# Kernel optimization log

Hardware: AMD Instinct MI355X
Metric: run time of the kernel (lower is better)

## Reference

```python
import jax, jax.numpy as jnp
import numpy as np
from jax import lax

V, E, H = 32000, 256, 512
B, S_SRC, S_TGT = 32, 128, 64


def setup_inputs() -> dict:
    key = jax.random.key(0)
    ks = jax.random.split(key, 16)
    n = lambda k, shp: jax.random.normal(k, shp, dtype=jnp.float32) * 0.05
    return {
        "src": jax.random.randint(ks[0], (B, S_SRC), 0, V, dtype=jnp.int32),
        "tgt": jax.random.randint(ks[1], (B, S_TGT), 0, V, dtype=jnp.int32),
        "enc_emb": n(ks[2], (V, E)),
        "enc_Wih": n(ks[3], (4 * H, E)),
        "enc_Whh": n(ks[4], (4 * H, H)),
        "enc_b": n(ks[5], (4 * H,)),
        "attn_W": n(ks[6], (H, 2 * H)),
        "attn_b": n(ks[7], (H,)),
        "attn_v": jax.random.uniform(ks[8], (H,), dtype=jnp.float32),
        "dec_emb": n(ks[9], (V, E)),
        "dec_Wih": n(ks[10], (4 * H, E + H)),
        "dec_Whh": n(ks[11], (4 * H, H)),
        "dec_b": n(ks[12], (4 * H,)),
        "out_W": n(ks[13], (V, H)),
        "out_b": n(ks[14], (V,)),
    }


def _lstm_cell(x, h, c, Wih, Whh, b):
    # PyTorch gate order: i, f, g, o. b = b_ih + b_hh fused.
    z = x @ Wih.T + h @ Whh.T + b  # [B, 4H]
    i, f, g, o = jnp.split(z, 4, axis=-1)
    c_new = jax.nn.sigmoid(f) * c + jax.nn.sigmoid(i) * jnp.tanh(g)
    h_new = jax.nn.sigmoid(o) * jnp.tanh(c_new)
    return h_new, c_new


def reference(src, tgt, enc_emb, enc_Wih, enc_Whh, enc_b, attn_W, attn_b,
              attn_v, dec_emb, dec_Wih, dec_Whh, dec_b, out_W, out_b):
    b = src.shape[0]
    h0 = jnp.zeros((b, H), dtype=enc_emb.dtype)
    c0 = jnp.zeros((b, H), dtype=enc_emb.dtype)

    # ---- Encoder: single-layer LSTM over src ----
    emb_src = enc_emb[src]  # [B, S_src, E]

    def enc_step(carry, x_t):
        h, c = carry
        h, c = _lstm_cell(x_t, h, c, enc_Wih, enc_Whh, enc_b)
        return (h, c), h

    (h, c), enc_out = lax.scan(enc_step, (h0, c0), emb_src.transpose(1, 0, 2))
    enc_out = enc_out.transpose(1, 0, 2)  # [B, S_src, H]

    # attn_W acts on cat([hidden, enc]); split into hidden and encoder parts.
    W_h = attn_W[:, :H]   # [H, H]
    W_e = attn_W[:, H:]   # [H, H]
    enc_proj = jnp.einsum('bsh,kh->bsk', enc_out, W_e)  # precomputed [B, S, H]

    # ---- Decoder with per-step Bahdanau attention ----
    emb_tgt = dec_emb[tgt].transpose(1, 0, 2)  # [T, B, E]

    def dec_step(carry, e_t):
        h, c = carry
        energy = jnp.tanh(enc_proj + (h @ W_h.T + attn_b)[:, None, :])  # [B,S,H]
        score = energy @ attn_v                                          # [B,S]
        a = jax.nn.softmax(score, axis=1)
        context = jnp.einsum('bs,bsh->bh', a, enc_out)                   # [B,H]
        x = jnp.concatenate([e_t, context], axis=-1)                     # [B,E+H]
        h, c = _lstm_cell(x, h, c, dec_Wih, dec_Whh, dec_b)
        return (h, c), h

    _, dec_h = lax.scan(dec_step, (h, c), emb_tgt)
    dec_h = dec_h.transpose(1, 0, 2)  # [B, T, H]

    return dec_h @ out_W.T + out_b  # [B, T, V]
```

## Files before the change

### kernel.cpp

```cpp
#include <hip/hip_runtime.h>

#define B_    32
#define SSRC  128
#define STGT  64
#define E_    256
#define H_    512
#define G4    2048
#define V_    32000

typedef unsigned short u16;
typedef unsigned long long u64b;
typedef short bf16x8 __attribute__((ext_vector_type(8)));
typedef float f32x4 __attribute__((ext_vector_type(4)));

__device__ __forceinline__ u16 f2b(float f) {
  unsigned u = __float_as_uint(f);
  u += 0x7FFFu + ((u >> 16) & 1u);
  return (u16)(u >> 16);
}
__device__ __forceinline__ float b2f(u16 h) {
  return __uint_as_float(((unsigned)h) << 16);
}
__device__ __forceinline__ unsigned pk2(float lo, float hi) {
  return (unsigned)f2b(lo) | (((unsigned)f2b(hi)) << 16);
}
__device__ __forceinline__ float sigm(float x) { return 1.0f / (1.0f + __expf(-x)); }
__device__ __forceinline__ float tanh_(float x) { return 1.0f - 2.0f / (1.0f + __expf(2.0f * x)); }

#if defined(__has_builtin)
#if __has_builtin(__builtin_amdgcn_fdot2_f32_bf16)
#define HAS_DOT2 1
#endif
#endif
#ifdef HAS_DOT2
typedef __bf16 b162 __attribute__((ext_vector_type(2)));
__device__ __forceinline__ float dot2u(unsigned a, unsigned b, float acc) {
  return __builtin_amdgcn_fdot2_f32_bf16(__builtin_bit_cast(b162, a),
                                         __builtin_bit_cast(b162, b), acc, false);
}
#else
__device__ __forceinline__ float dot2u(unsigned a, unsigned b, float acc) {
  acc += __uint_as_float(a << 16) * __uint_as_float(b << 16);
  acc += __uint_as_float(a & 0xffff0000u) * __uint_as_float(b & 0xffff0000u);
  return acc;
}
#endif
__device__ __forceinline__ float dot4(uint4 w, uint4 h, float acc) {
  return dot2u(w.w, h.w, dot2u(w.z, h.z, dot2u(w.y, h.y, dot2u(w.x, h.x, acc))));
}

__device__ __forceinline__ int swz64(int c) {
  return (c & ~3) | ((c & 3) ^ ((c >> 3) & 3));
}

__device__ __forceinline__ uint4 cload4(const void* p) {
  uint4 r;
  asm volatile("global_load_dwordx4 %0, %1, off sc0 sc1\n\ts_waitcnt vmcnt(0)"
               : "=&v"(r) : "v"(p) : "memory");
  return r;
}
__device__ __forceinline__ void cstoref(float* p, float v) {
  asm volatile("global_store_dword %0, %1, off sc0 sc1" :: "v"(p), "v"(v) : "memory");
}
__device__ __forceinline__ void cstoreu(unsigned* p, unsigned v) {
  asm volatile("global_store_dword %0, %1, off sc0 sc1" :: "v"(p), "v"(v) : "memory");
}
__device__ __forceinline__ float cloadf_relaxed(const float* p) {
  return __hip_atomic_load(p, __ATOMIC_RELAXED, __HIP_MEMORY_SCOPE_AGENT);
}

__device__ __forceinline__ void arrive(int* flags, int myid, int target) {
  asm volatile("s_waitcnt vmcnt(0)" ::: "memory");
  __syncthreads();
  if (threadIdx.x == 0)
    __hip_atomic_store(flags + myid, target, __ATOMIC_RELAXED, __HIP_MEMORY_SCOPE_AGENT);
}
__device__ __forceinline__ void waitbar(int* flags, int target) {
  if (threadIdx.x < 64) {
    int l = threadIdx.x & 31;
    while (__hip_atomic_load(flags + l, __ATOMIC_RELAXED, __HIP_MEMORY_SCOPE_AGENT) < target)
      __builtin_amdgcn_s_sleep(1);
  }
  __syncthreads();
  asm volatile("" ::: "memory");
}

__global__ void prep_kernel(const int* __restrict__ src, const int* __restrict__ tgt,
                            const float* __restrict__ enc_emb, const float* __restrict__ dec_emb,
                            const float* __restrict__ enc_Wih, const float* __restrict__ dec_Wih,
                            const float* __restrict__ out_W,
                            u16* __restrict__ A_enc, u16* __restrict__ A_dec,
                            u16* __restrict__ WihE, u16* __restrict__ WihD,
                            u16* __restrict__ WihC, u16* __restrict__ outWb)
{
  const long n_outw = (long)V_ * H_;
  const long n_aenc = (long)B_ * SSRC * E_;
  const long n_adec = (long)B_ * STGT * E_;
  const long n_wih  = (long)G4 * E_;
  const long n_wcp  = (long)G4 * H_;
  const long total = n_outw + n_aenc + n_adec + 2 * n_wih + n_wcp;
  for (long i = (long)blockIdx.x * blockDim.x + threadIdx.x; i < total;
       i += (long)gridDim.x * blockDim.x) {
    long x = i;
    if (x < n_outw) { outWb[x] = f2b(out_W[x]); continue; }
    x -= n_outw;
    if (x < n_aenc) {
      int row = (int)(x >> 8), e = (int)(x & 255);
      A_enc[x] = f2b(enc_emb[(size_t)src[row] * E_ + e]);
      continue;
    }
    x -= n_aenc;
    if (x < n_adec) {
      int row = (int)(x >> 8), e = (int)(x & 255);
      A_dec[x] = f2b(dec_emb[(size_t)tgt[row] * E_ + e]);
      continue;
    }
    x -= n_adec;
    if (x < n_wih) { WihE[x] = f2b(enc_Wih[x]); continue; }
    x -= n_wih;
    if (x < n_wih) {
      int r = (int)(x >> 8), e = (int)(x & 255);
      WihD[x] = f2b(dec_Wih[(size_t)r * 768 + e]);
      continue;
    }
    x -= n_wih;
    {
      int r = (int)(x >> 9), k = (int)(x & 511);
      WihC[x] = f2b(dec_Wih[(size_t)r * 768 + 256 + k]);
    }
  }
}

template<int KTOT, bool OBF>
__global__ __launch_bounds__(256, 2) void gemm_nt(
    const u16* __restrict__ A, const u16* __restrict__ Bm,
    const float* __restrict__ bias, void* __restrict__ Cv, int M, int N)
{
  int nbm = M >> 7;
  int bn = blockIdx.x / nbm;
  int bm = blockIdx.x % nbm;
  int w = threadIdx.x >> 6, l = threadIdx.x & 63;
  int wr = w >> 1, wc = w & 1;
  int m0 = bm * 128 + wr * 64, n0 = bn * 128 + wc * 64;
  int lr = l & 15, ko = (l >> 4) * 8;
  f32x4 acc[4][4] = {};
  const u16* Ap = A + (size_t)(m0 + lr) * KTOT + ko;
  const u16* Bp = Bm + (size_t)(n0 + lr) * KTOT + ko;
  for (int k0 = 0; k0 < KTOT; k0 += 32) {
    bf16x8 af[4], bfr[4];
#pragma unroll
    for (int i = 0; i < 4; ++i) af[i] = *(const bf16x8*)(Ap + (size_t)i * 16 * KTOT + k0);
#pragma unroll
    for (int i = 0; i < 4; ++i) bfr[i] = *(const bf16x8*)(Bp + (size_t)i * 16 * KTOT + k0);
#pragma unroll
    for (int i = 0; i < 4; ++i)
#pragma unroll
      for (int j = 0; j < 4; ++j)
        acc[i][j] = __builtin_amdgcn_mfma_f32_16x16x32_bf16(af[i], bfr[j], acc[i][j], 0, 0, 0);
  }
  int rbase = (l >> 4) * 4;
#pragma unroll
  for (int i = 0; i < 4; ++i) {
#pragma unroll
    for (int j = 0; j < 4; ++j) {
      int gn = n0 + j * 16 + lr;
      float bv = bias[gn];
#pragma unroll
      for (int r = 0; r < 4; ++r) {
        int gm = m0 + i * 16 + rbase + r;
        float v = acc[i][j][r] + bv;
        if (OBF) ((u16*)Cv)[(size_t)gm * N + gn] = f2b(v);
        else     ((float*)Cv)[(size_t)gm * N + gn] = v;
      }
    }
  }
}

__device__ __forceinline__ void zgemv64(int tid, const uint4* Wu, const uint4* Hu,
                                        float (*part)[64][4]) {
  int rq = tid >> 4, kq = tid & 15;
  float acc[4][4] = {};
#pragma unroll
  for (int u = 0; u < 4; ++u) {
    int sc = swz64(kq * 4 + u);
    uint4 h0 = Hu[sc], h1 = Hu[64 + sc], h2 = Hu[128 + sc], h3 = Hu[192 + sc];
#pragma unroll
    for (int r = 0; r < 4; ++r) {
      uint4 wv = Wu[(rq * 4 + r) * 64 + sc];
      acc[r][0] = dot4(wv, h0, acc[r][0]);
      acc[r][1] = dot4(wv, h1, acc[r][1]);
      acc[r][2] = dot4(wv, h2, acc[r][2]);
      acc[r][3] = dot4(wv, h3, acc[r][3]);
    }
  }
#pragma unroll
  for (int r = 0; r < 4; ++r) {
    float4 v = {acc[r][0], acc[r][1], acc[r][2], acc[r][3]};
    *(float4*)&part[kq][(rq * 4 + r) ^ (kq & 7)][0] = v;
  }
}

template<typename GrowF>
__device__ __forceinline__ void fillw64(int tid, const float* Wsrc, uint4* Wu, GrowF grow) {
#pragma unroll 4
  for (int i = 0; i < 16; ++i) {
    int idx4 = tid + i * 256;
    int row = idx4 >> 6, c = idx4 & 63;
    const float* s = Wsrc + (size_t)grow(row) * 512 + c * 8;
    float4 a = *(const float4*)s, b4 = *(const float4*)(s + 4);
    uint4 pkv = {pk2(a.x, a.y), pk2(a.z, a.w), pk2(b4.x, b4.y), pk2(b4.z, b4.w)};
    Wu[row * 64 + swz64(c)] = pkv;
  }
}

__global__ __launch_bounds__(256, 1) void encoder_kernel(
    const float* __restrict__ enc_Whh, const float* __restrict__ attn_W,
    const u16* __restrict__ WihC, const u16* __restrict__ encXW,
    unsigned* __restrict__ h16buf, float* __restrict__ cfin,
    u16* __restrict__ eprojb, u16* __restrict__ eoPw, int* __restrict__ bars)
{
  const int tid = threadIdx.x;
  const int g = blockIdx.x & 7;
  const int gb = blockIdx.x >> 3;
  const int b0 = g * 4;
  const int ds0 = gb * 16;
  int* flags = bars + g * 64;

  __shared__ uint4 encW4[64 * 64];
  __shared__ uint4 web4[16 * 64];
  __shared__ uint4 hl16[4 * 64];
  __shared__ float part[16][64][4];
  __shared__ float zx[4][64];
  __shared__ float cS[4][16];

  if (tid < 64) cS[tid >> 4][tid & 15] = 0.f;
  fillw64(tid, enc_Whh, encW4, [&](int row) { return (row >> 4) * 512 + ds0 + (row & 15); });
#pragma unroll
  for (int i = 0; i < 4; ++i) {
    int idx4 = tid + i * 256;
    int row = idx4 >> 6, c = idx4 & 63;
    const float* s = attn_W + (size_t)(ds0 + row) * 1024 + 512 + c * 8;
    float4 a = *(const float4*)s, b4 = *(const float4*)(s + 4);
    uint4 pkv = {pk2(a.x, a.y), pk2(a.z, a.w), pk2(b4.x, b4.y), pk2(b4.z, b4.w)};
    web4[row * 64 + (c ^ (row & 7))] = pkv;
  }
  __syncthreads();

  for (int t = 0; t < SSRC; ++t) {
    {
      int row = tid >> 6, c = tid & 63;
      uint4 v = cload4((const uint4*)h16buf + (size_t)(t & 1) * 2048 + (b0 + row) * 64 + c);
      hl16[row * 64 + swz64(c)] = v;
    }
    __syncthreads();
    zgemv64(tid, encW4, hl16, part);
    __syncthreads();
    {
      int b_l = tid >> 6, rl = tid & 63;
      float z = 0.f;
#pragma unroll
      for (int kq = 0; kq < 16; ++kq) z += part[kq][rl ^ (kq & 7)][b_l];
      int grow = (rl >> 4) * 512 + ds0 + (rl & 15);
      z += b2f(encXW[((size_t)(b0 + b_l) * SSRC + t) * G4 + grow]);
      zx[b_l][rl] = z;
    }
    __syncthreads();
    if (tid < 64) {
      int bl = tid >> 4, jl = tid & 15;
      float iv = zx[bl][jl], fv = zx[bl][16 + jl], gv = zx[bl][32 + jl], ov = zx[bl][48 + jl];
      float cn = sigm(fv) * cS[bl][jl] + sigm(iv) * tanh_(gv);
      float hn = sigm(ov) * tanh_(cn);
      cS[bl][jl] = cn;
      float hn1 = __shfl_down(hn, 1);
      if ((jl & 1) == 0)
        cstoreu(h16buf + (size_t)((t + 1) & 1) * 8192 + (size_t)(b0 + bl) * 256 + gb * 8 + (jl >> 1),
                pk2(hn, hn1));
    }
    arrive(flags, gb, t + 1);
    if (t > 0) {
      int tm1 = t - 1;
      {
        int d_l = tid >> 4, b_l = (tid >> 2) & 3, kq4 = tid & 3;
        float acc = 0.f;
#pragma unroll
        for (int u = 0; u < 16; ++u) {
          int c = kq4 * 16 + u;
          acc = dot4(web4[d_l * 64 + (c ^ (d_l & 7))], hl16[b_l * 64 + swz64(c)], acc);
        }
        acc += __shfl_xor(acc, 1);
        acc += __shfl_xor(acc, 2);
        if (kq4 == 0)
          eprojb[(((size_t)(b0 + b_l) * SSRC + tm1) << 9) + ds0 + d_l] = f2b(acc);
      }
      {
        int r = tid >> 2, kq4 = tid & 3;
        int n = (r >> 4) * 512 + ds0 + (r & 15);
        const uint4* wr_ = (const uint4*)(WihC + (size_t)n * 512) + kq4 * 16;
        float a0 = 0.f, a1 = 0.f, a2 = 0.f, a3 = 0.f;
#pragma unroll
        for (int u = 0; u < 16; ++u) {
          uint4 wv = wr_[u];
          int sc = swz64(kq4 * 16 + u);
          a0 = dot4(wv, hl16[sc], a0);
          a1 = dot4(wv, hl16[64 + sc], a1);
          a2 = dot4(wv, hl16[128 + sc], a2);
          a3 = dot4(wv, hl16[192 + sc], a3);
        }
        a0 += __shfl_xor(a0, 1); a0 += __shfl_xor(a0, 2);
        a1 += __shfl_xor(a1, 1); a1 += __shfl_xor(a1, 2);
        a2 += __shfl_xor(a2, 1); a2 += __shfl_xor(a2, 2);
        a3 += __shfl_xor(a3, 1); a3 += __shfl_xor(a3, 2);
        if (kq4 == 0) {
          size_t base = ((size_t)b0 * SSRC + tm1) << 11;
          eoPw[base + n] = f2b(a0);
          eoPw[base + (SSRC << 11) + n] = f2b(a1);
          eoPw[base + (2u * SSRC << 11) + n] = f2b(a2);
          eoPw[base + (3u * SSRC << 11) + n] = f2b(a3);
        }
      }
    }
    waitbar(flags, t + 1);
  }
  {
    int row = tid >> 6, c = tid & 63;
    uint4 v = cload4((const uint4*)h16buf + (b0 + row) * 64 + c);
    hl16[row * 64 + swz64(c)] = v;
  }
  __syncthreads();
  {
    int tm1 = SSRC - 1;
    {
      int d_l = tid >> 4, b_l = (tid >> 2) & 3, kq4 = tid & 3;
      float acc = 0.f;
#pragma unroll
      for (int u = 0; u < 16; ++u) {
        int c = kq4 * 16 + u;
        acc = dot4(web4[d_l * 64 + (c ^ (d_l & 7))], hl16[b_l * 64 + swz64(c)], acc);
      }
      acc += __shfl_xor(acc, 1);
      acc += __shfl_xor(acc, 2);
      if (kq4 == 0)
        eprojb[(((size_t)(b0 + b_l) * SSRC + tm1) << 9) + ds0 + d_l] = f2b(acc);
    }
    {
      int r = tid >> 2, kq4 = tid & 3;
      int n = (r >> 4) * 512 + ds0 + (r & 15);
      const uint4* wr_ = (const uint4*)(WihC + (size_t)n * 512) + kq4 * 16;
      float a0 = 0.f, a1 = 0.f, a2 = 0.f, a3 = 0.f;
#pragma unroll
      for (int u = 0; u < 16; ++u) {
        uint4 wv = wr_[u];
        int sc = swz64(kq4 * 16 + u);
        a0 = dot4(wv, hl16[sc], a0);
        a1 = dot4(wv, hl16[64 + sc], a1);
        a2 = dot4(wv, hl16[128 + sc], a2);
        a3 = dot4(wv, hl16[192 + sc], a3);
      }
      a0 += __shfl_xor(a0, 1); a0 += __shfl_xor(a0, 2);
      a1 += __shfl_xor(a1, 1); a1 += __shfl_xor(a1, 2);
      a2 += __shfl_xor(a2, 1); a2 += __shfl_xor(a2, 2);
      a3 += __shfl_xor(a3, 1); a3 += __shfl_xor(a3, 2);
      if (kq4 == 0) {
        size_t base = ((size_t)b0 * SSRC + tm1) << 11;
        eoPw[base + n] = f2b(a0);
        eoPw[base + (SSRC << 11) + n] = f2b(a1);
        eoPw[base + (2u * SSRC << 11) + n] = f2b(a2);
        eoPw[base + (3u * SSRC << 11) + n] = f2b(a3);
      }
    }
  }
  if (tid < 64)
    cfin[(size_t)(b0 + (tid >> 4)) * H_ + ds0 + (tid & 15)] = cS[tid >> 4][tid & 15];
}

__global__ __launch_bounds__(256, 1) void decoder_kernel(
    const float* __restrict__ dec_Whh, const float* __restrict__ attn_W,
    const float* __restrict__ attn_b, const float* __restrict__ attn_v,
    const u16* __restrict__ eprojb, const u16* __restrict__ decXW,
    const u16* __restrict__ eoPb,
    unsigned* __restrict__ hd16, const float* __restrict__ cfin,
    float* __restrict__ vpart ,
    u16* __restrict__ dech, int* __restrict__ bars)
{
  const int tid = threadIdx.x;
  const int g = blockIdx.x & 7;
  const int gb = blockIdx.x >> 3;
  const int b0 = g * 4;
  const int ds0 = gb * 16;
  int* flags = bars + g * 64;
  int ep_ = 0;

  __shared__ uint4 decW4[64 * 64];
  __shared__ uint4 Whb4[16 * 64];
  __shared__ uint4 hl16[4 * 64];
  __shared__ float part[16][64][4];
  __shared__ float partE[8][64][4];
  __shared__ float scoreS[4][128];
  __shared__ float aS[4][128];
  __shared__ float zx[4][64];
  __shared__ float qS[4][16];
  __shared__ float cS[4][16];
  __shared__ float vS[16], bS[16];

  if (tid < 64) cS[tid >> 4][tid & 15] = cfin[(size_t)(b0 + (tid >> 4)) * H_ + ds0 + (tid & 15)];
  if (tid < 16) { vS[tid] = attn_v[ds0 + tid]; bS[tid] = attn_b[ds0 + tid]; }
  fillw64(tid, dec_Whh, decW4, [&](int row) { return (row >> 4) * 512 + ds0 + (row & 15); });
#pragma unroll
  for (int i = 0; i < 4; ++i) {
    int idx4 = tid + i * 256;
    int row = idx4 >> 6, c = idx4 & 63;
    const float* s = attn_W + (size_t)(ds0 + row) * 1024 + c * 8;
    float4 a = *(const float4*)s, b4 = *(const float4*)(s + 4);
    uint4 pkv = {pk2(a.x, a.y), pk2(a.z, a.w), pk2(b4.x, b4.y), pk2(b4.z, b4.w)};
    Whb4[row * 64 + (c ^ (row & 7))] = pkv;
  }
  const int sq = tid >> 5, cp = tid & 31;
  const int n32 = (cp >> 3) * 256 + gb * 8 + (cp & 7);
  uint4 eor[16];
  {
    const unsigned* eoPu = (const unsigned*)eoPb;
#pragma unroll
    for (int si = 0; si < 16; ++si) {
      int s = sq * 16 + si;
      eor[si].x = eoPu[((size_t)(b0 + 0) * SSRC + s) * 1024 + n32];
      eor[si].y = eoPu[((size_t)(b0 + 1) * SSRC + s) * 1024 + n32];
      eor[si].z = eoPu[((size_t)(b0 + 2) * SSRC + s) * 1024 + n32];
      eor[si].w = eoPu[((size_t)(b0 + 3) * SSRC + s) * 1024 + n32];
    }
  }
  __syncthreads();

  for (int t = 0; t < STGT; ++t) {
    {
      int row = tid >> 6, c = tid & 63;
      uint4 v = cload4((const uint4*)hd16 + (b0 + row) * 64 + c);
      hl16[row * 64 + swz64(c)] = v;
    }
    __syncthreads();
    {
      int b_l = tid >> 6, d_l = (tid >> 2) & 15, kq4 = tid & 3;
      float acc = 0.f;
#pragma unroll
      for (int u = 0; u < 16; ++u) {
        int c = kq4 * 16 + u;
        acc = dot4(Whb4[d_l * 64 + (c ^ (d_l & 7))], hl16[b_l * 64 + swz64(c)], acc);
      }
      acc += __shfl_xor(acc, 1);
      acc += __shfl_xor(acc, 2);
      if (kq4 == 0) qS[b_l][d_l] = acc + bS[d_l];
    }
    __syncthreads();
    {
      float* vp = vpart + ((size_t)g * 32 + gb) * 512;
#pragma unroll
      for (int r = 0; r < 2; ++r) {
        int idx = tid + r * 256;
        int b_l = idx >> 7, s = idx & 127;
        const uint4* ep = (const uint4*)(eprojb + (((size_t)(b0 + b_l) * SSRC + s) << 9) + ds0);
        uint4 e0 = ep[0], e1 = ep[1];
        float acc = 0.f;
        acc += vS[0]  * tanh_(b2f((u16)(e0.x & 0xffff)) + qS[b_l][0]);
        acc += vS[1]  * tanh_(b2f((u16)(e0.x >> 16))    + qS[b_l][1]);
        acc += vS[2]  * tanh_(b2f((u16)(e0.y & 0xffff)) + qS[b_l][2]);
        acc += vS[3]  * tanh_(b2f((u16)(e0.y >> 16))    + qS[b_l][3]);
        acc += vS[4]  * tanh_(b2f((u16)(e0.z & 0xffff)) + qS[b_l][4]);
        acc += vS[5]  * tanh_(b2f((u16)(e0.z >> 16))    + qS[b_l][5]);
        acc += vS[6]  * tanh_(b2f((u16)(e0.w & 0xffff)) + qS[b_l][6]);
        acc += vS[7]  * tanh_(b2f((u16)(e0.w >> 16))    + qS[b_l][7]);
        acc += vS[8]  * tanh_(b2f((u16)(e1.x & 0xffff)) + qS[b_l][8]);
        acc += vS[9]  * tanh_(b2f((u16)(e1.x >> 16))    + qS[b_l][9]);
        acc += vS[10] * tanh_(b2f((u16)(e1.y & 0xffff)) + qS[b_l][10]);
        acc += vS[11] * tanh_(b2f((u16)(e1.y >> 16))    + qS[b_l][11]);
        acc += vS[12] * tanh_(b2f((u16)(e1.z & 0xffff)) + qS[b_l][12]);
        acc += vS[13] * tanh_(b2f((u16)(e1.z >> 16))    + qS[b_l][13]);
        acc += vS[14] * tanh_(b2f((u16)(e1.w & 0xffff)) + qS[b_l][14]);
        acc += vS[15] * tanh_(b2f((u16)(e1.w >> 16))    + qS[b_l][15]);
        cstoref(vp + idx, acc);
      }
    }
    arrive(flags, gb, ++ep_);
    zgemv64(tid, decW4, hl16, part);
    waitbar(flags, ep_);

    {
      int b_l = tid >> 6, s0 = (tid & 63) * 2;
      float a0 = 0.f, a1 = 0.f;
#pragma unroll 8
      for (int j = 0; j < 32; ++j) {
        const float* p = vpart + ((size_t)g * 32 + j) * 512 + b_l * 128 + s0;
        a0 += cloadf_relaxed(p);
        a1 += cloadf_relaxed(p + 1);
      }
      scoreS[b_l][s0] = a0;
      scoreS[b_l][s0 + 1] = a1;
    }
    __syncthreads();
    {
      int w = tid >> 6, lane = tid & 63;
      float s1 = scoreS[w][lane], s2v = scoreS[w][64 + lane];
      float m = fmaxf(s1, s2v);
#pragma unroll
      for (int off = 32; off; off >>= 1) m = fmaxf(m, __shfl_xor(m, off));
      float e1 = __expf(s1 - m), e2 = __expf(s2v - m);
      float sm = e1 + e2;
#pragma unroll
      for (int off = 32; off; off >>= 1) sm += __shfl_xor(sm, off);
      float inv = 1.0f / sm;
      aS[w][lane] = e1 * inv;
      aS[w][64 + lane] = e2 * inv;
    }
    __syncthreads();
    {
      float a0 = 0.f, a1 = 0.f, a2 = 0.f, a3 = 0.f, a4 = 0.f, a5 = 0.f, a6 = 0.f, a7 = 0.f;
#pragma unroll
      for (int si = 0; si < 16; ++si) {
        int s = sq * 16 + si;
        float w0 = aS[0][s], w1 = aS[1][s], w2 = aS[2][s], w3 = aS[3][s];
        unsigned u0 = eor[si].x, u1 = eor[si].y, u2 = eor[si].z, u3 = eor[si].w;
        a0 += w0 * b2f((u16)(u0 & 0xffff)); a1 += w0 * b2f((u16)(u0 >> 16));
        a2 += w1 * b2f((u16)(u1 & 0xffff)); a3 += w1 * b2f((u16)(u1 >> 16));
        a4 += w2 * b2f((u16)(u2 & 0xffff)); a5 += w2 * b2f((u16)(u2 >> 16));
        a6 += w3 * b2f((u16)(u3 & 0xffff)); a7 += w3 * b2f((u16)(u3 >> 16));
      }
      int r0 = (cp >> 3) * 16 + (cp & 7) * 2;
      float4 lo = {a0, a2, a4, a6}, hi = {a1, a3, a5, a7};
      *(float4*)&partE[sq][r0][0] = lo;
      *(float4*)&partE[sq][r0 + 1][0] = hi;
    }
    __syncthreads();
    {
      int b_l = tid >> 6, rl = tid & 63;
      float z = 0.f;
#pragma unroll
      for (int kq = 0; kq < 16; ++kq) z += part[kq][rl ^ (kq & 7)][b_l];
#pragma unroll
      for (int sq2 = 0; sq2 < 8; ++sq2) z += partE[sq2][rl][b_l];
      int grow = (rl >> 4) * 512 + ds0 + (rl & 15);
      z += b2f(decXW[((size_t)(b0 + b_l) * STGT + t) * G4 + grow]);
      zx[b_l][rl] = z;
    }
    __syncthreads();
    if (tid < 64) {
      int bl = tid >> 4, jl = tid & 15;
      float iv = zx[bl][jl], fv = zx[bl][16 + jl], gv = zx[bl][32 + jl], ov = zx[bl][48 + jl];
      float cn = sigm(fv) * cS[bl][jl] + sigm(iv) * tanh_(gv);
      float hn = sigm(ov) * tanh_(cn);
      cS[bl][jl] = cn;
      dech[((size_t)(b0 + bl) * STGT + t) * H_ + ds0 + jl] = f2b(hn);
      float hn1 = __shfl_down(hn, 1);
      if ((jl & 1) == 0)
        cstoreu(hd16 + (size_t)(b0 + bl) * 256 + gb * 8 + (jl >> 1), pk2(hn, hn1));
    }
    arrive(flags, gb, ++ep_);
    waitbar(flags, ep_);
  }
}

#define OFF_BARE   0u
#define OFF_BARD   2048u
#define OFF_H16    4096u
#define OFF_CFIN   69632u
#define OFF_VPART  135168u
#define OFF_AENC   1048576u
#define OFF_ADEC   3145728u
#define OFF_WIHE   4194304u
#define OFF_WIHD   5242880u
#define OFF_WIHC   6291456u
#define OFF_OUTW   8388608u
#define OFF_ENCXW  41943040u
#define OFF_DECXW  58720256u
#define OFF_EPROJ  67108864u
#define OFF_DECH   71303168u

extern "C" void kernel_launch(void* const* d_in, const int* in_sizes, int n_in,
                              void* d_out, int out_size, void* d_ws, size_t ws_size,
                              hipStream_t stream)
{
  const int*   src     = (const int*)d_in[0];
  const int*   tgt     = (const int*)d_in[1];
  const float* enc_emb = (const float*)d_in[2];
  const float* enc_Wih = (const float*)d_in[3];
  const float* enc_Whh = (const float*)d_in[4];
  const float* enc_b   = (const float*)d_in[5];
  const float* attn_W  = (const float*)d_in[6];
  const float* attn_b  = (const float*)d_in[7];
  const float* attn_v  = (const float*)d_in[8];
  const float* dec_emb = (const float*)d_in[9];
  const float* dec_Wih = (const float*)d_in[10];
  const float* dec_Whh = (const float*)d_in[11];
  const float* dec_b   = (const float*)d_in[12];
  const float* out_W   = (const float*)d_in[13];
  const float* out_b   = (const float*)d_in[14];

  char* ws = (char*)d_ws;
  int*      barE   = (int*)(ws + OFF_BARE);
  int*      barD   = (int*)(ws + OFF_BARD);
  unsigned* h16buf = (unsigned*)(ws + OFF_H16);
  float*    cfin   = (float*)(ws + OFF_CFIN);
  float*    vpart  = (float*)(ws + OFF_VPART);
  u16*      A_enc  = (u16*)(ws + OFF_AENC);
  u16*      A_dec  = (u16*)(ws + OFF_ADEC);
  u16*      WihE   = (u16*)(ws + OFF_WIHE);
  u16*      WihD   = (u16*)(ws + OFF_WIHD);
  u16*      WihC   = (u16*)(ws + OFF_WIHC);
  u16*      outWb  = (u16*)(ws + OFF_OUTW);
  u16*      encXW  = (u16*)(ws + OFF_ENCXW);
  u16*      eoPb   = (u16*)(ws + OFF_ENCXW);
  u16*      decXW  = (u16*)(ws + OFF_DECXW);
  u16*      eprojb = (u16*)(ws + OFF_EPROJ);
  u16*      dech   = (u16*)(ws + OFF_DECH);

  (void)hipMemsetAsync(d_ws, 0, OFF_H16 + 65536, stream);

  prep_kernel<<<2048, 256, 0, stream>>>(src, tgt, enc_emb, dec_emb, enc_Wih, dec_Wih,
                                        out_W, A_enc, A_dec, WihE, WihD, WihC, outWb);

  gemm_nt<256, true><<<512, 256, 0, stream>>>(A_enc, WihE, enc_b, (void*)encXW, 4096, 2048);
  gemm_nt<256, true><<<256, 256, 0, stream>>>(A_dec, WihD, dec_b, (void*)decXW, 2048, 2048);

  encoder_kernel<<<256, 256, 0, stream>>>(enc_Whh, attn_W, WihC, encXW,
                                          h16buf, cfin, eprojb, eoPb, barE);

  decoder_kernel<<<256, 256, 0, stream>>>(dec_Whh, attn_W, attn_b, attn_v,
                                          eprojb, decXW, eoPb, h16buf, cfin,
                                          vpart, dech, barD);

  gemm_nt<512, false><<<4000, 256, 0, stream>>>(dech, outWb, out_b, d_out, 2048, 32000);
}
```

Measured before the change: 1.735 ms.

## Move encoder-output projections out of recurrent loop into batched MFMA GEMMs

The encoder kernel no longer computes the attention key projection and the decoder context-weight projection per timestep with scalar dot products between barriers. It now writes encoder hidden states to global memory, and two MFMA GEMMs compute both projections in bulk afterwards, with the context-weight rows pre-permuted so the decoder can index them contiguously. The decoder also caches its slice of the projected keys in shared memory instead of reloading them from global memory every step, and the per-step input-projection load is hoisted ahead of the barrier wait. This shortens each serial encoder step at the cost of two extra kernel launches and an extra round trip of the encoder outputs through global memory.

```diff
diff --git a/kernel.cpp b/kernel.cpp
--- a/kernel.cpp
+++ b/kernel.cpp
@@ -9,7 +9,6 @@
 #define V_    32000
 
 typedef unsigned short u16;
-typedef unsigned long long u64b;
 typedef short bf16x8 __attribute__((ext_vector_type(8)));
 typedef float f32x4 __attribute__((ext_vector_type(4)));
 
@@ -84,21 +83,27 @@
   __syncthreads();
   asm volatile("" ::: "memory");
 }
+__device__ __forceinline__ void gbar(int* flags, int myid, int target) {
+  arrive(flags, myid, target);
+  waitbar(flags, target);
+}
 
 __global__ void prep_kernel(const int* __restrict__ src, const int* __restrict__ tgt,
                             const float* __restrict__ enc_emb, const float* __restrict__ dec_emb,
                             const float* __restrict__ enc_Wih, const float* __restrict__ dec_Wih,
-                            const float* __restrict__ out_W,
+                            const float* __restrict__ attn_W, const float* __restrict__ out_W,
                             u16* __restrict__ A_enc, u16* __restrict__ A_dec,
                             u16* __restrict__ WihE, u16* __restrict__ WihD,
-                            u16* __restrict__ WihC, u16* __restrict__ outWb)
+                            u16* __restrict__ Web, u16* __restrict__ WihCp,
+                            u16* __restrict__ outWb)
 {
   const long n_outw = (long)V_ * H_;
   const long n_aenc = (long)B_ * SSRC * E_;
   const long n_adec = (long)B_ * STGT * E_;
   const long n_wih  = (long)G4 * E_;
+  const long n_web  = (long)H_ * H_;
   const long n_wcp  = (long)G4 * H_;
-  const long total = n_outw + n_aenc + n_adec + 2 * n_wih + n_wcp;
+  const long total = n_outw + n_aenc + n_adec + 2 * n_wih + n_web + n_wcp;
   for (long i = (long)blockIdx.x * blockDim.x + threadIdx.x; i < total;
        i += (long)gridDim.x * blockDim.x) {
     long x = i;
@@ -124,9 +129,17 @@
       continue;
     }
     x -= n_wih;
-    {
-      int r = (int)(x >> 9), k = (int)(x & 511);
-      WihC[x] = f2b(dec_Wih[(size_t)r * 768 + 256 + k]);
+    if (x < n_web) {
+      int d = (int)(x >> 9), k = (int)(x & 511);
+      Web[x] = f2b(attn_W[(size_t)d * 1024 + 512 + k]);
+      continue;
+    }
+    x -= n_web;
+    {
+      int n = (int)(x >> 9), k = (int)(x & 511);
+      int gb = n >> 6, gate = (n >> 4) & 3, jl = n & 15;
+      int orig = gate * 512 + gb * 16 + jl;
+      WihCp[x] = f2b(dec_Wih[(size_t)orig * 768 + 256 + k]);
     }
   }
 }
@@ -164,7 +177,7 @@
 #pragma unroll
     for (int j = 0; j < 4; ++j) {
       int gn = n0 + j * 16 + lr;
-      float bv = bias[gn];
+      float bv = bias ? bias[gn] : 0.f;
 #pragma unroll
       for (int r = 0; r < 4; ++r) {
         int gm = m0 + i * 16 + rbase + r;
@@ -214,10 +227,9 @@
 }
 
 __global__ __launch_bounds__(256, 1) void encoder_kernel(
-    const float* __restrict__ enc_Whh, const float* __restrict__ attn_W,
-    const u16* __restrict__ WihC, const u16* __restrict__ encXW,
-    unsigned* __restrict__ h16buf, float* __restrict__ cfin,
-    u16* __restrict__ eprojb, u16* __restrict__ eoPw, int* __restrict__ bars)
+    const float* __restrict__ enc_Whh, const u16* __restrict__ encXW,
+    unsigned* __restrict__ h16buf ,
+    float* __restrict__ cfin, u16* __restrict__ eo_g, int* __restrict__ bars)
 {
   const int tid = threadIdx.x;
   const int g = blockIdx.x & 7;
@@ -227,7 +239,6 @@
   int* flags = bars + g * 64;
 
   __shared__ uint4 encW4[64 * 64];
-  __shared__ uint4 web4[16 * 64];
   __shared__ uint4 hl16[4 * 64];
   __shared__ float part[16][64][4];
   __shared__ float zx[4][64];
@@ -235,18 +246,14 @@
 
   if (tid < 64) cS[tid >> 4][tid & 15] = 0.f;
   fillw64(tid, enc_Whh, encW4, [&](int row) { return (row >> 4) * 512 + ds0 + (row & 15); });
-#pragma unroll
-  for (int i = 0; i < 4; ++i) {
-    int idx4 = tid + i * 256;
-    int row = idx4 >> 6, c = idx4 & 63;
-    const float* s = attn_W + (size_t)(ds0 + row) * 1024 + 512 + c * 8;
-    float4 a = *(const float4*)s, b4 = *(const float4*)(s + 4);
-    uint4 pkv = {pk2(a.x, a.y), pk2(a.z, a.w), pk2(b4.x, b4.y), pk2(b4.z, b4.w)};
-    web4[row * 64 + (c ^ (row & 7))] = pkv;
-  }
   __syncthreads();
 
+  const int bl_c = tid >> 6, rl_c = tid & 63;
+  const int grow_c = (rl_c >> 4) * 512 + ds0 + (rl_c & 15);
+  const u16* xwp = encXW + (size_t)(b0 + bl_c) * SSRC * G4 + grow_c;
+
   for (int t = 0; t < SSRC; ++t) {
+    u16 xw = xwp[(size_t)t * G4];
     {
       int row = tid >> 6, c = tid & 63;
       uint4 v = cload4((const uint4*)h16buf + (size_t)(t & 1) * 2048 + (b0 + row) * 64 + c);
@@ -256,13 +263,11 @@
     zgemv64(tid, encW4, hl16, part);
     __syncthreads();
     {
-      int b_l = tid >> 6, rl = tid & 63;
       float z = 0.f;
 #pragma unroll
-      for (int kq = 0; kq < 16; ++kq) z += part[kq][rl ^ (kq & 7)][b_l];
-      int grow = (rl >> 4) * 512 + ds0 + (rl & 15);
-      z += b2f(encXW[((size_t)(b0 + b_l) * SSRC + t) * G4 + grow]);
-      zx[b_l][rl] = z;
+      for (int kq = 0; kq < 16; ++kq) z += part[kq][rl_c ^ (kq & 7)][bl_c];
+      z += b2f(xw);
+      zx[bl_c][rl_c] = z;
     }
     __syncthreads();
     if (tid < 64) {
@@ -271,103 +276,13 @@
       float cn = sigm(fv) * cS[bl][jl] + sigm(iv) * tanh_(gv);
       float hn = sigm(ov) * tanh_(cn);
       cS[bl][jl] = cn;
+      eo_g[((size_t)(b0 + bl) * SSRC + t) * H_ + ds0 + jl] = f2b(hn);
       float hn1 = __shfl_down(hn, 1);
       if ((jl & 1) == 0)
         cstoreu(h16buf + (size_t)((t + 1) & 1) * 8192 + (size_t)(b0 + bl) * 256 + gb * 8 + (jl >> 1),
                 pk2(hn, hn1));
     }
-    arrive(flags, gb, t + 1);
-    if (t > 0) {
-      int tm1 = t - 1;
-      {
-        int d_l = tid >> 4, b_l = (tid >> 2) & 3, kq4 = tid & 3;
-        float acc = 0.f;
-#pragma unroll
-        for (int u = 0; u < 16; ++u) {
-          int c = kq4 * 16 + u;
-          acc = dot4(web4[d_l * 64 + (c ^ (d_l & 7))], hl16[b_l * 64 + swz64(c)], acc);
-        }
-        acc += __shfl_xor(acc, 1);
-        acc += __shfl_xor(acc, 2);
-        if (kq4 == 0)
-          eprojb[(((size_t)(b0 + b_l) * SSRC + tm1) << 9) + ds0 + d_l] = f2b(acc);
-      }
-      {
-        int r = tid >> 2, kq4 = tid & 3;
-        int n = (r >> 4) * 512 + ds0 + (r & 15);
-        const uint4* wr_ = (const uint4*)(WihC + (size_t)n * 512) + kq4 * 16;
-        float a0 = 0.f, a1 = 0.f, a2 = 0.f, a3 = 0.f;
-#pragma unroll
-        for (int u = 0; u < 16; ++u) {
-          uint4 wv = wr_[u];
-          int sc = swz64(kq4 * 16 + u);
-          a0 = dot4(wv, hl16[sc], a0);
-          a1 = dot4(wv, hl16[64 + sc], a1);
-          a2 = dot4(wv, hl16[128 + sc], a2);
-          a3 = dot4(wv, hl16[192 + sc], a3);
-        }
-        a0 += __shfl_xor(a0, 1); a0 += __shfl_xor(a0, 2);
-        a1 += __shfl_xor(a1, 1); a1 += __shfl_xor(a1, 2);
-        a2 += __shfl_xor(a2, 1); a2 += __shfl_xor(a2, 2);
-        a3 += __shfl_xor(a3, 1); a3 += __shfl_xor(a3, 2);
-        if (kq4 == 0) {
-          size_t base = ((size_t)b0 * SSRC + tm1) << 11;
-          eoPw[base + n] = f2b(a0);
-          eoPw[base + (SSRC << 11) + n] = f2b(a1);
-          eoPw[base + (2u * SSRC << 11) + n] = f2b(a2);
-          eoPw[base + (3u * SSRC << 11) + n] = f2b(a3);
-        }
-      }
-    }
-    waitbar(flags, t + 1);
-  }
-  {
-    int row = tid >> 6, c = tid & 63;
-    uint4 v = cload4((const uint4*)h16buf + (b0 + row) * 64 + c);
-    hl16[row * 64 + swz64(c)] = v;
-  }
-  __syncthreads();
-  {
-    int tm1 = SSRC - 1;
-    {
-      int d_l = tid >> 4, b_l = (tid >> 2) & 3, kq4 = tid & 3;
-      float acc = 0.f;
-#pragma unroll
-      for (int u = 0; u < 16; ++u) {
-        int c = kq4 * 16 + u;
-        acc = dot4(web4[d_l * 64 + (c ^ (d_l & 7))], hl16[b_l * 64 + swz64(c)], acc);
-      }
-      acc += __shfl_xor(acc, 1);
-      acc += __shfl_xor(acc, 2);
-      if (kq4 == 0)
-        eprojb[(((size_t)(b0 + b_l) * SSRC + tm1) << 9) + ds0 + d_l] = f2b(acc);
-    }
-    {
-      int r = tid >> 2, kq4 = tid & 3;
-      int n = (r >> 4) * 512 + ds0 + (r & 15);
-      const uint4* wr_ = (const uint4*)(WihC + (size_t)n * 512) + kq4 * 16;
-      float a0 = 0.f, a1 = 0.f, a2 = 0.f, a3 = 0.f;
-#pragma unroll
-      for (int u = 0; u < 16; ++u) {
-        uint4 wv = wr_[u];
-        int sc = swz64(kq4 * 16 + u);
-        a0 = dot4(wv, hl16[sc], a0);
-        a1 = dot4(wv, hl16[64 + sc], a1);
-        a2 = dot4(wv, hl16[128 + sc], a2);
-        a3 = dot4(wv, hl16[192 + sc], a3);
-      }
-      a0 += __shfl_xor(a0, 1); a0 += __shfl_xor(a0, 2);
-      a1 += __shfl_xor(a1, 1); a1 += __shfl_xor(a1, 2);
-      a2 += __shfl_xor(a2, 1); a2 += __shfl_xor(a2, 2);
-      a3 += __shfl_xor(a3, 1); a3 += __shfl_xor(a3, 2);
-      if (kq4 == 0) {
-        size_t base = ((size_t)b0 * SSRC + tm1) << 11;
-        eoPw[base + n] = f2b(a0);
-        eoPw[base + (SSRC << 11) + n] = f2b(a1);
-        eoPw[base + (2u * SSRC << 11) + n] = f2b(a2);
-        eoPw[base + (3u * SSRC << 11) + n] = f2b(a3);
-      }
-    }
+    gbar(flags, gb, t + 1);
   }
   if (tid < 64)
     cfin[(size_t)(b0 + (tid >> 4)) * H_ + ds0 + (tid & 15)] = cS[tid >> 4][tid & 15];
@@ -392,6 +307,7 @@
 
   __shared__ uint4 decW4[64 * 64];
   __shared__ uint4 Whb4[16 * 64];
+  __shared__ uint4 epL[512][2];
   __shared__ uint4 hl16[4 * 64];
   __shared__ float part[16][64][4];
   __shared__ float partE[8][64][4];
@@ -414,8 +330,16 @@
     uint4 pkv = {pk2(a.x, a.y), pk2(a.z, a.w), pk2(b4.x, b4.y), pk2(b4.z, b4.w)};
     Whb4[row * 64 + (c ^ (row & 7))] = pkv;
   }
+#pragma unroll
+  for (int r = 0; r < 2; ++r) {
+    int idx = tid + r * 256;
+    int b_l = idx >> 7, s = idx & 127;
+    const uint4* ep = (const uint4*)(eprojb + (((size_t)(b0 + b_l) * SSRC + s) << 9) + ds0);
+    epL[idx][0] = ep[0];
+    epL[idx][1] = ep[1];
+  }
   const int sq = tid >> 5, cp = tid & 31;
-  const int n32 = (cp >> 3) * 256 + gb * 8 + (cp & 7);
+  const int n32 = gb * 32 + cp;
   uint4 eor[16];
   {
     const unsigned* eoPu = (const unsigned*)eoPb;
@@ -430,7 +354,12 @@
   }
   __syncthreads();
 
+  const int bl_c = tid >> 6, rl_c = tid & 63;
+  const int grow_c = (rl_c >> 4) * 512 + ds0 + (rl_c & 15);
+  const u16* xwp = decXW + (size_t)(b0 + bl_c) * STGT * G4 + grow_c;
+
   for (int t = 0; t < STGT; ++t) {
+    u16 xw = xwp[(size_t)t * G4];
     {
       int row = tid >> 6, c = tid & 63;
       uint4 v = cload4((const uint4*)hd16 + (b0 + row) * 64 + c);
@@ -455,9 +384,8 @@
 #pragma unroll
       for (int r = 0; r < 2; ++r) {
         int idx = tid + r * 256;
-        int b_l = idx >> 7, s = idx & 127;
-        const uint4* ep = (const uint4*)(eprojb + (((size_t)(b0 + b_l) * SSRC + s) << 9) + ds0);
-        uint4 e0 = ep[0], e1 = ep[1];
+        int b_l = idx >> 7;
+        uint4 e0 = epL[idx][0], e1 = epL[idx][1];
         float acc = 0.f;
         acc += vS[0]  * tanh_(b2f((u16)(e0.x & 0xffff)) + qS[b_l][0]);
         acc += vS[1]  * tanh_(b2f((u16)(e0.x >> 16))    + qS[b_l][1]);
@@ -522,22 +450,20 @@
         a4 += w2 * b2f((u16)(u2 & 0xffff)); a5 += w2 * b2f((u16)(u2 >> 16));
         a6 += w3 * b2f((u16)(u3 & 0xffff)); a7 += w3 * b2f((u16)(u3 >> 16));
       }
-      int r0 = (cp >> 3) * 16 + (cp & 7) * 2;
+      int r0 = cp * 2;
       float4 lo = {a0, a2, a4, a6}, hi = {a1, a3, a5, a7};
       *(float4*)&partE[sq][r0][0] = lo;
       *(float4*)&partE[sq][r0 + 1][0] = hi;
     }
     __syncthreads();
     {
-      int b_l = tid >> 6, rl = tid & 63;
       float z = 0.f;
 #pragma unroll
-      for (int kq = 0; kq < 16; ++kq) z += part[kq][rl ^ (kq & 7)][b_l];
-#pragma unroll
-      for (int sq2 = 0; sq2 < 8; ++sq2) z += partE[sq2][rl][b_l];
-      int grow = (rl >> 4) * 512 + ds0 + (rl & 15);
-      z += b2f(decXW[((size_t)(b0 + b_l) * STGT + t) * G4 + grow]);
-      zx[b_l][rl] = z;
+      for (int kq = 0; kq < 16; ++kq) z += part[kq][rl_c ^ (kq & 7)][bl_c];
+#pragma unroll
+      for (int sq2 = 0; sq2 < 8; ++sq2) z += partE[sq2][rl_c][bl_c];
+      z += b2f(xw);
+      zx[bl_c][rl_c] = z;
     }
     __syncthreads();
     if (tid < 64) {
@@ -561,16 +487,18 @@
 #define OFF_H16    4096u
 #define OFF_CFIN   69632u
 #define OFF_VPART  135168u
-#define OFF_AENC   1048576u
-#define OFF_ADEC   3145728u
-#define OFF_WIHE   4194304u
-#define OFF_WIHD   5242880u
-#define OFF_WIHC   6291456u
-#define OFF_OUTW   8388608u
-#define OFF_ENCXW  41943040u
-#define OFF_DECXW  58720256u
-#define OFF_EPROJ  67108864u
-#define OFF_DECH   71303168u
+#define OFF_AENC   659456u
+#define OFF_ADEC   2756608u
+#define OFF_WIHE   3805184u
+#define OFF_WIHD   4853760u
+#define OFF_WEB    5902336u
+#define OFF_WIHCP  6426624u
+#define OFF_OUTW   8523776u
+#define OFF_ENCXW  41291776u
+#define OFF_DECXW  58068992u
+#define OFF_EO     66457600u
+#define OFF_EPROJ  70651904u
+#define OFF_DECH   74846208u
 
 extern "C" void kernel_launch(void* const* d_in, const int* in_sizes, int n_in,
                               void* d_out, int out_size, void* d_ws, size_t ws_size,
@@ -602,24 +530,28 @@
   u16*      A_dec  = (u16*)(ws + OFF_ADEC);
   u16*      WihE   = (u16*)(ws + OFF_WIHE);
   u16*      WihD   = (u16*)(ws + OFF_WIHD);
-  u16*      WihC   = (u16*)(ws + OFF_WIHC);
+  u16*      Web    = (u16*)(ws + OFF_WEB);
+  u16*      WihCp  = (u16*)(ws + OFF_WIHCP);
   u16*      outWb  = (u16*)(ws + OFF_OUTW);
   u16*      encXW  = (u16*)(ws + OFF_ENCXW);
   u16*      eoPb   = (u16*)(ws + OFF_ENCXW);
   u16*      decXW  = (u16*)(ws + OFF_DECXW);
+  u16*      eo_g   = (u16*)(ws + OFF_EO);
   u16*      eprojb = (u16*)(ws + OFF_EPROJ);
   u16*      dech   = (u16*)(ws + OFF_DECH);
 
   (void)hipMemsetAsync(d_ws, 0, OFF_H16 + 65536, stream);
 
   prep_kernel<<<2048, 256, 0, stream>>>(src, tgt, enc_emb, dec_emb, enc_Wih, dec_Wih,
-                                        out_W, A_enc, A_dec, WihE, WihD, WihC, outWb);
+                                        attn_W, out_W, A_enc, A_dec, WihE, WihD, Web, WihCp, outWb);
 
   gemm_nt<256, true><<<512, 256, 0, stream>>>(A_enc, WihE, enc_b, (void*)encXW, 4096, 2048);
   gemm_nt<256, true><<<256, 256, 0, stream>>>(A_dec, WihD, dec_b, (void*)decXW, 2048, 2048);
 
-  encoder_kernel<<<256, 256, 0, stream>>>(enc_Whh, attn_W, WihC, encXW,
-                                          h16buf, cfin, eprojb, eoPb, barE);
+  encoder_kernel<<<256, 256, 0, stream>>>(enc_Whh, encXW, h16buf, cfin, eo_g, barE);
+
+  gemm_nt<512, true><<<128, 256, 0, stream>>>(eo_g, Web, nullptr, (void*)eprojb, 4096, 512);
+  gemm_nt<512, true><<<512, 256, 0, stream>>>(eo_g, WihCp, nullptr, (void*)eoPb, 4096, 2048);
 
   decoder_kernel<<<256, 256, 0, stream>>>(dec_Whh, attn_W, attn_b, attn_v,
                                           eprojb, decXW, eoPb, h16buf, cfin,
```

New measurement: 1.388 ms, median of 2. 1.25x faster.
